# Optimization experiments

Measured on AMD Instinct MI355X. Metric: run time of the kernel, lower is better.

## Reference

```python
import jax, jax.numpy as jnp
import numpy as np

N_A = 50000; N_B = 50000          # nodes per type
FD = 8; BINS = 32; EMB = 16       # discrete features, bins, per-feature embed dim
HID = 64; ZD = 32                 # hidden_dim, embed_dim
E = 800000                        # edges per relation (avg degree 16)


def setup_inputs() -> dict:
    key = jax.random.key(0)
    ks = iter(jax.random.split(key, 64))
    def nrm(shape, s=0.05):
        return jax.random.normal(next(ks), shape, jnp.float32) * s
    def ri(shape, hi):
        return jax.random.randint(next(ks), shape, 0, hi, dtype=jnp.int32)
    inp = {
        'x_A': ri((N_A, FD), BINS),
        'x_B': ri((N_B, FD), BINS),
        'ei_ab': ri((2, E), N_A),   # src in A, dst in B (N_A == N_B)
        'ei_ba': ri((2, E), N_B),
        'ei_aa': ri((2, E), N_A),
        # per-feature embedding tables [FD, BINS, EMB]
        'emb_A': nrm((FD, BINS, EMB)), 'emb_B': nrm((FD, BINS, EMB)),
        # pre_lin per node type (in = FD*EMB)
        'pre_W_A': nrm((FD * EMB, HID)), 'pre_b_A': nrm((HID,)),
        'pre_W_B': nrm((FD * EMB, HID)), 'pre_b_B': nrm((HID,)),
        # SAGEConv per relation: lin_l (on aggregated msgs, with bias), lin_r (root, no bias)
        'sage_l_W_ab': nrm((HID, HID)), 'sage_l_b_ab': nrm((HID,)), 'sage_r_W_ab': nrm((HID, HID)),
        'sage_l_W_ba': nrm((HID, HID)), 'sage_l_b_ba': nrm((HID,)), 'sage_r_W_ba': nrm((HID, HID)),
        'sage_l_W_aa': nrm((HID, HID)), 'sage_l_b_aa': nrm((HID,)), 'sage_r_W_aa': nrm((HID, HID)),
        # lin_proj per node type
        'proj_W_A': nrm((HID, ZD)), 'proj_b_A': nrm((ZD,)),
        'proj_W_B': nrm((HID, ZD)), 'proj_b_B': nrm((ZD,)),
        # feature heads per node type -> FD*BINS logits
        'head_W_A': nrm((ZD, FD * BINS)), 'head_b_A': nrm((FD * BINS,)),
        'head_W_B': nrm((ZD, FD * BINS)), 'head_b_B': nrm((FD * BINS,)),
        # bilinear edge decoders per relation: W [1, ZD, ZD], bias [1]
        'bil_W_ab': nrm((1, ZD, ZD)), 'bil_b_ab': nrm((1,)),
        'bil_W_ba': nrm((1, ZD, ZD)), 'bil_b_ba': nrm((1,)),
        'bil_W_aa': nrm((1, ZD, ZD)), 'bil_b_aa': nrm((1,)),
    }
    return inp


def _segment_mean(vals, idx, n):
    s = jax.ops.segment_sum(vals, idx, num_segments=n)
    c = jax.ops.segment_sum(jnp.ones((vals.shape[0], 1), vals.dtype), idx, num_segments=n)
    return s / jnp.maximum(c, 1.0)


def _sage(x_src, x_dst, ei, Wl, bl, Wr):
    # SAGEConv: lin_l(mean_{j in N(i)} x_j) + lin_r(x_i)
    m = _segment_mean(x_src[ei[0]], ei[1], x_dst.shape[0])
    return m @ Wl + bl + x_dst @ Wr


def _embed(x, emb):
    # emb: [FD, BINS, EMB]; x: [N, FD] ints -> [N, FD*EMB]
    e = emb[jnp.arange(FD)[None, :], x]            # [N, FD, EMB]
    return e.reshape(x.shape[0], FD * EMB)


def _bilinear(zs, zd, W, b):
    # nn.Bilinear: out_o = zs^T W_o zd + b_o ; here out dim 1, squeeze
    return (jnp.einsum('ei,oij,ej->eo', zs, W, zd) + b)[:, 0]


def _forward(x_A, x_B, ei_ab, ei_ba, ei_aa,
             emb_A, emb_B, pre_W_A, pre_b_A, pre_W_B, pre_b_B,
             sage_l_W_ab, sage_l_b_ab, sage_r_W_ab,
             sage_l_W_ba, sage_l_b_ba, sage_r_W_ba,
             sage_l_W_aa, sage_l_b_aa, sage_r_W_aa,
             proj_W_A, proj_b_A, proj_W_B, proj_b_B,
             head_W_A, head_b_A, head_W_B, head_b_B,
             bil_W_ab, bil_b_ab, bil_W_ba, bil_b_ba, bil_W_aa, bil_b_aa):
    # feature encoder + pre_lin + relu
    x0_A = jax.nn.relu(_embed(x_A, emb_A) @ pre_W_A + pre_b_A)
    x0_B = jax.nn.relu(_embed(x_B, emb_B) @ pre_W_B + pre_b_B)
    # HeteroConv(SAGEConv per relation, aggr='mean' over relations per dst type)
    h_B = _sage(x0_A, x0_B, ei_ab, sage_l_W_ab, sage_l_b_ab, sage_r_W_ab)
    h_A = (_sage(x0_B, x0_A, ei_ba, sage_l_W_ba, sage_l_b_ba, sage_r_W_ba)
           + _sage(x0_A, x0_A, ei_aa, sage_l_W_aa, sage_l_b_aa, sage_r_W_aa)) * 0.5
    # projection
    z_A = jax.nn.relu(h_A @ proj_W_A + proj_b_A)
    z_B = jax.nn.relu(h_B @ proj_W_B + proj_b_B)
    # feature decode
    fl_A = (z_A @ head_W_A + head_b_A).reshape(-1, FD, BINS)
    fl_B = (z_B @ head_W_B + head_b_B).reshape(-1, FD, BINS)
    # edge decode (bilinear on gathered endpoint embeddings)
    s_ab = _bilinear(z_A[ei_ab[0]], z_B[ei_ab[1]], bil_W_ab, bil_b_ab)
    s_ba = _bilinear(z_B[ei_ba[0]], z_A[ei_ba[1]], bil_W_ba, bil_b_ba)
    s_aa = _bilinear(z_A[ei_aa[0]], z_A[ei_aa[1]], bil_W_aa, bil_b_aa)
    return (z_A, z_B, fl_A, fl_B, s_ab, s_ba, s_aa)


def reference(x_A, x_B, ei_ab, ei_ba, ei_aa,
              emb_A, emb_B, pre_W_A, pre_b_A, pre_W_B, pre_b_B,
              sage_l_W_ab, sage_l_b_ab, sage_r_W_ab,
              sage_l_W_ba, sage_l_b_ba, sage_r_W_ba,
              sage_l_W_aa, sage_l_b_aa, sage_r_W_aa,
              proj_W_A, proj_b_A, proj_W_B, proj_b_B,
              head_W_A, head_b_A, head_W_B, head_b_B,
              bil_W_ab, bil_b_ab, bil_W_ba, bil_b_ba, bil_W_aa, bil_b_aa):
    return _forward(x_A, x_B, ei_ab, ei_ba, ei_aa,
                    emb_A, emb_B, pre_W_A, pre_b_A, pre_W_B, pre_b_B,
                    sage_l_W_ab, sage_l_b_ab, sage_r_W_ab,
                    sage_l_W_ba, sage_l_b_ba, sage_r_W_ba,
                    sage_l_W_aa, sage_l_b_aa, sage_r_W_aa,
                    proj_W_A, proj_b_A, proj_W_B, proj_b_B,
                    head_W_A, head_b_A, head_W_B, head_b_B,
                    bil_W_ab, bil_b_ab, bil_W_ba, bil_b_ba, bil_W_aa, bil_b_aa)
```

## Files before the change

### kernel.cpp

```cpp
#include <hip/hip_runtime.h>

typedef unsigned short u16;
typedef unsigned int u32;
typedef __attribute__((ext_vector_type(8))) short short8;
typedef __attribute__((ext_vector_type(4))) float f32x4;

constexpr int NA = 50000, NB = 50000;
constexpr int EMB = 16, HID = 64;
constexpr int NE = 800000;
constexpr int NBKT = 782;
constexpr int CAPB = 1536;
constexpr int EPB = 2048;
constexpr int BPR = (NE + EPB - 1) / EPB;
constexpr int MSB = 3 * BPR;

#define MFMA16(a, b, c) __builtin_amdgcn_mfma_f32_16x16x32_bf16(a, b, c, 0, 0, 0)

__device__ inline u16 f2bf(float f) {
  u32 b = __float_as_uint(f);
  return (u16)((b + 0x7FFFu + ((b >> 16) & 1u)) >> 16);
}
__device__ inline float bfl(u32 u) { return __uint_as_float(u << 16); }
__device__ inline float bfh(u32 u) { return __uint_as_float(u & 0xFFFF0000u); }
__device__ inline float bfs(u16 u) { return __uint_as_float((u32)u << 16); }

__global__ void __launch_bounds__(256) k_pre(
    const float* __restrict__ embA, const float* __restrict__ embB,
    const float* __restrict__ preWA, const float* __restrict__ preWB,
    float* __restrict__ T,
    const float* __restrict__ Wr_ba, const float* __restrict__ Wr_aa,
    const float* __restrict__ Wl_ba, const float* __restrict__ Wl_aa,
    const float* __restrict__ Wl_ab, const float* __restrict__ Wr_ab,
    const float* __restrict__ bl_ba, const float* __restrict__ bl_aa,
    const float* __restrict__ projWA, const float* __restrict__ projWB,
    const float* __restrict__ headWA, const float* __restrict__ headWB,
    const float* __restrict__ bilW_ba, const float* __restrict__ bilW_aa,
    const float* __restrict__ bilW_ab,
    u16* __restrict__ frag, float* __restrict__ bhA,
    const int* __restrict__ ei_ab, const int* __restrict__ ei_ba,
    const int* __restrict__ ei_aa, int* __restrict__ gcur,
    u32* __restrict__ buckets) {
  __shared__ int hist[NBKT];
  __shared__ int wcur[NBKT];
  int blk = blockIdx.x;
  int t = threadIdx.x;

  if (blk < MSB) {
    int rel = blk / BPR;
    int lb = blk - rel * BPR;
    const int* ei = rel == 0 ? ei_ab : (rel == 1 ? ei_ba : ei_aa);
    int e0 = lb * EPB;
    int n = min(EPB, NE - e0);
    for (int i = t; i < NBKT; i += 256) hist[i] = 0;
    __syncthreads();
    for (int i = t; i < n; i += 256) {
      int dstn = ei[NE + e0 + i];
      atomicAdd(&hist[dstn >> 6], 1);
    }
    __syncthreads();
    for (int i = t; i < NBKT; i += 256) {
      int c = hist[i];
      wcur[i] = (c > 0) ? atomicAdd(&gcur[rel * NBKT + i], c) : 0;
    }
    __syncthreads();
    for (int i = t; i < n; i += 256) {
      int src = ei[e0 + i];
      int dstn = ei[NE + e0 + i];
      int b = dstn >> 6;
      int pos = atomicAdd(&wcur[b], 1);
      if (pos < CAPB)
        buckets[(size_t)(rel * NBKT + b) * CAPB + pos] =
            ((u32)src << 6) | (u32)(dstn & 63);
    }
    return;
  }

  if (blk < MSB + 128) {
    int id = (blk - MSB) * 256 + t;
    int type = id >> 14;
    int rem = id & 16383;
    int col = rem >> 8;
    int fdbin = rem & 255;
    int fd = fdbin >> 5;
    const float* emb = type ? embB : embA;
    const float* W = type ? preWB : preWA;
    const float* e = emb + fdbin * EMB;
    const float* w = W + (fd * EMB) * HID + col;
    float s = 0.f;
#pragma unroll
    for (int j = 0; j < EMB; ++j) s += e[j] * w[j * HID];
    T[id] = s;
    return;
  }

  int tid = (blk - MSB - 128) * 256 + t;
  if (tid >= 86 * 64) {
    int i = tid - 86 * 64;
    if (i < 64) bhA[i] = 0.5f * (bl_ba[i] + bl_aa[i]);
    return;
  }
  int f = tid >> 6, lane = tid & 63;
  int nidx = lane & 15, quad = lane >> 4;
  u16* dst = frag + (size_t)f * 512 + lane * 8;
#pragma unroll
  for (int j = 0; j < 8; ++j) {
    int kq = quad * 8 + j;
    float v;
    if (f < 24) {
      int s = f >> 2, nt = f & 3, k = s * 32 + kq, c = nt * 16 + nidx;
      v = (k < 64) ? 0.5f * (Wr_ba[k * 64 + c] + Wr_aa[k * 64 + c])
          : (k < 128) ? 0.5f * Wl_ba[(k - 64) * 64 + c]
                      : 0.5f * Wl_aa[(k - 128) * 64 + c];
    } else if (f < 28) {
      int g = f - 24, k = (g >> 1) * 32 + kq, c = (g & 1) * 16 + nidx;
      v = projWA[k * 32 + c];
    } else if (f < 44) {
      int c = (f - 28) * 16 + nidx;
      v = headWA[kq * 256 + c];
    } else if (f < 46) {
      int i2 = (f - 44) * 16 + nidx;
      v = bilW_ba[i2 * 32 + kq];
    } else if (f < 48) {
      int i2 = (f - 46) * 16 + nidx;
      v = bilW_aa[i2 * 32 + kq];
    } else if (f < 64) {
      int g = f - 48, s = g >> 2, nt = g & 3, k = s * 32 + kq, c = nt * 16 + nidx;
      v = (k < 64) ? Wr_ab[k * 64 + c] : Wl_ab[(k - 64) * 64 + c];
    } else if (f < 68) {
      int g = f - 64, k = (g >> 1) * 32 + kq, c = (g & 1) * 16 + nidx;
      v = projWB[k * 32 + c];
    } else if (f < 84) {
      int c = (f - 68) * 16 + nidx;
      v = headWB[kq * 256 + c];
    } else {
      int i2 = (f - 84) * 16 + nidx;
      v = bilW_ab[i2 * 32 + kq];
    }
    dst[j] = f2bf(v);
  }
}

__global__ void __launch_bounds__(256) k_x0(const int* __restrict__ xA,
                                            const int* __restrict__ xB,
                                            const float* __restrict__ T,
                                            const float* __restrict__ biasA,
                                            const float* __restrict__ biasB,
                                            u16* __restrict__ x0A,
                                            u16* __restrict__ x0B) {
  extern __shared__ float Tl[];
  int blk = blockIdx.x;
  int type = blk >= 782;
  int lb = type ? blk - 782 : blk;
  const int* x = type ? xB : xA;
  const float* Tt = T + (type ? 16384 : 0);
  const float* bias = type ? biasB : biasA;
  u16* x0 = type ? x0B : x0A;
  const int N = NA;

  const float4* Tg = (const float4*)Tt;
  float4* Ts = (float4*)Tl;
  for (int i = threadIdx.x; i < 4096; i += 256) {
    int col = i >> 6, b4 = i & 63;
    Ts[col * 64 + ((b4 + 2 * (col >> 4)) & 63)] = Tg[i];
  }
  __syncthreads();
  int t = threadIdx.x;
  int r = t >> 2, q = t & 3;
  int row = lb * 64 + r;
  bool valid = row < N;
  int arow = valid ? row : (N - 1);
  const int4* xp = (const int4*)(x + arow * 8);
  int4 xa = xp[0], xb = xp[1];
  int bins[8] = {xa.x, xa.y, xa.z, xa.w, xb.x, xb.y, xb.z, xb.w};
  int c0 = q * 16;
  float acc[16];
#pragma unroll
  for (int j = 0; j < 16; ++j) acc[j] = bias[c0 + j];
#pragma unroll
  for (int fd = 0; fd < 8; ++fd) {
    int sb = ((fd * 32 + bins[fd]) + 8 * q) & 255;
#pragma unroll
    for (int j = 0; j < 16; ++j) acc[j] += Tl[(c0 + j) * 256 + sb];
  }
  if (valid) {
    u32 p[8];
#pragma unroll
    for (int j = 0; j < 8; ++j) {
      u16 lo = f2bf(fmaxf(acc[2 * j], 0.f));
      u16 hi = f2bf(fmaxf(acc[2 * j + 1], 0.f));
      p[j] = (u32)lo | ((u32)hi << 16);
    }
    u32* o = (u32*)(x0 + (size_t)row * 64 + c0);
    *(uint4*)o = *(uint4*)&p[0];
    *((uint4*)o + 1) = *(uint4*)&p[4];
  }
}

__global__ void __launch_bounds__(256) k_meansort_all(
    const u32* __restrict__ buckets, const int* __restrict__ cur,
    const u16* __restrict__ x0A, const u16* __restrict__ x0B,
    u16* __restrict__ mab, u16* __restrict__ mba, u16* __restrict__ maa) {
  __shared__ u32 ebuf[CAPB];
  __shared__ u16 csr[CAPB];
  __shared__ int dcnt[64], doff[64], wcur[64];
  int blk = blockIdx.x;
  int rel = blk / NBKT;
  int lb = blk - rel * NBKT;
  int t = threadIdx.x;
  const u16* x0 = (rel == 1) ? x0B : x0A;
  u16* out = rel == 0 ? mab : (rel == 1 ? mba : maa);
  int n = min(cur[blk], CAPB);
  const u32* bk = buckets + (size_t)blk * CAPB;
  if (t < 64) dcnt[t] = 0;
  __syncthreads();
  for (int i = t; i < n; i += 256) {
    u32 v = bk[i];
    ebuf[i] = v;
    atomicAdd(&dcnt[v & 63], 1);
  }
  __syncthreads();
  if (t == 0) {
    int s = 0;
#pragma unroll
    for (int d = 0; d < 64; ++d) {
      doff[d] = s;
      wcur[d] = s;
      s += dcnt[d];
    }
  }
  __syncthreads();
  for (int i = t; i < n; i += 256) {
    u32 v = ebuf[i];
    int p = atomicAdd(&wcur[v & 63], 1);
    csr[p] = (u16)(v >> 6);
  }
  __syncthreads();
  int lane = t & 63, w = t >> 6;
  int g = lane >> 4;
  int dim4 = (lane & 15) * 4;
  int base = lb * 64;
  for (int c = 0; c < 4; ++c) {
    int dloc = w * 16 + c * 4 + g;
    int dstn = base + dloc;
    if (dstn < 50000) {
      int off = doff[dloc], deg = dcnt[dloc];
      float a0 = 0.f, a1 = 0.f, a2 = 0.f, a3 = 0.f;
      int i = 0;
      for (; i + 8 <= deg; i += 8) {
        uint2 v0 = *(const uint2*)(x0 + (size_t)csr[off + i] * 64 + dim4);
        uint2 v1 = *(const uint2*)(x0 + (size_t)csr[off + i + 1] * 64 + dim4);
        uint2 v2 = *(const uint2*)(x0 + (size_t)csr[off + i + 2] * 64 + dim4);
        uint2 v3 = *(const uint2*)(x0 + (size_t)csr[off + i + 3] * 64 + dim4);
        uint2 v4 = *(const uint2*)(x0 + (size_t)csr[off + i + 4] * 64 + dim4);
        uint2 v5 = *(const uint2*)(x0 + (size_t)csr[off + i + 5] * 64 + dim4);
        uint2 v6 = *(const uint2*)(x0 + (size_t)csr[off + i + 6] * 64 + dim4);
        uint2 v7 = *(const uint2*)(x0 + (size_t)csr[off + i + 7] * 64 + dim4);
        a0 += bfl(v0.x) + bfl(v1.x) + bfl(v2.x) + bfl(v3.x) +
              bfl(v4.x) + bfl(v5.x) + bfl(v6.x) + bfl(v7.x);
        a1 += bfh(v0.x) + bfh(v1.x) + bfh(v2.x) + bfh(v3.x) +
              bfh(v4.x) + bfh(v5.x) + bfh(v6.x) + bfh(v7.x);
        a2 += bfl(v0.y) + bfl(v1.y) + bfl(v2.y) + bfl(v3.y) +
              bfl(v4.y) + bfl(v5.y) + bfl(v6.y) + bfl(v7.y);
        a3 += bfh(v0.y) + bfh(v1.y) + bfh(v2.y) + bfh(v3.y) +
              bfh(v4.y) + bfh(v5.y) + bfh(v6.y) + bfh(v7.y);
      }
      for (; i + 4 <= deg; i += 4) {
        uint2 v0 = *(const uint2*)(x0 + (size_t)csr[off + i] * 64 + dim4);
        uint2 v1 = *(const uint2*)(x0 + (size_t)csr[off + i + 1] * 64 + dim4);
        uint2 v2 = *(const uint2*)(x0 + (size_t)csr[off + i + 2] * 64 + dim4);
        uint2 v3 = *(const uint2*)(x0 + (size_t)csr[off + i + 3] * 64 + dim4);
        a0 += bfl(v0.x) + bfl(v1.x) + bfl(v2.x) + bfl(v3.x);
        a1 += bfh(v0.x) + bfh(v1.x) + bfh(v2.x) + bfh(v3.x);
        a2 += bfl(v0.y) + bfl(v1.y) + bfl(v2.y) + bfl(v3.y);
        a3 += bfh(v0.y) + bfh(v1.y) + bfh(v2.y) + bfh(v3.y);
      }
      for (; i < deg; ++i) {
        uint2 v0 = *(const uint2*)(x0 + (size_t)csr[off + i] * 64 + dim4);
        a0 += bfl(v0.x);
        a1 += bfh(v0.x);
        a2 += bfl(v0.y);
        a3 += bfh(v0.y);
      }
      float inv = deg > 0 ? 1.f / (float)deg : 0.f;
      uint2 o;
      o.x = (u32)f2bf(a0 * inv) | ((u32)f2bf(a1 * inv) << 16);
      o.y = (u32)f2bf(a2 * inv) | ((u32)f2bf(a3 * inv) << 16);
      *(uint2*)(out + (size_t)dstn * 64 + dim4) = o;
    }
  }
}

template <int NS, int NY>
__device__ __forceinline__ void node_chain(
    const u16* __restrict__ x0, const u16* __restrict__ m1, const u16* __restrict__ m2,
    const u16* __restrict__ frag, int f1, int f2, int fy, int fh,
    const float* __restrict__ hbias, const float* __restrict__ projb,
    const float* __restrict__ headb,
    float* __restrict__ zout, float* __restrict__ flout,
    u16* __restrict__ zbf, u16* __restrict__ y1bf, u16* __restrict__ y2bf,
    int rows0, int N, u16* hld, u16* zld, int lane) {
  int nidx = lane & 15, quad = lane >> 4;
  size_t r0 = (size_t)min(rows0 + nidx, N - 1);
  size_t r1 = (size_t)min(rows0 + 16 + nidx, N - 1);

  f32x4 acc[2][4];
#pragma unroll
  for (int mt = 0; mt < 2; ++mt)
#pragma unroll
    for (int nt = 0; nt < 4; ++nt) acc[mt][nt] = {0.f, 0.f, 0.f, 0.f};
  const u16* mats[3] = {x0, m1, m2};
#pragma unroll
  for (int s = 0; s < NS; ++s) {
    const u16* src = mats[s >> 1];
    int koff = (s & 1) * 32 + quad * 8;
    short8 a0 = *(const short8*)(src + r0 * 64 + koff);
    short8 a1 = *(const short8*)(src + r1 * 64 + koff);
#pragma unroll
    for (int nt = 0; nt < 4; ++nt) {
      short8 b = *(const short8*)(frag + (size_t)(f1 + s * 4 + nt) * 512 + lane * 8);
      acc[0][nt] = MFMA16(a0, b, acc[0][nt]);
      acc[1][nt] = MFMA16(a1, b, acc[1][nt]);
    }
  }
#pragma unroll
  for (int mt = 0; mt < 2; ++mt)
#pragma unroll
    for (int nt = 0; nt < 4; ++nt) {
      int col = nt * 16 + nidx;
      float bb = hbias[col];
#pragma unroll
      for (int r2 = 0; r2 < 4; ++r2)
        hld[(mt * 16 + quad * 4 + r2) * 72 + col] = f2bf(acc[mt][nt][r2] + bb);
    }

  f32x4 zacc[2][2];
#pragma unroll
  for (int mt = 0; mt < 2; ++mt)
#pragma unroll
    for (int nt = 0; nt < 2; ++nt) zacc[mt][nt] = {0.f, 0.f, 0.f, 0.f};
#pragma unroll
  for (int s = 0; s < 2; ++s) {
    short8 a0 = *(const short8*)(hld + nidx * 72 + s * 32 + quad * 8);
    short8 a1 = *(const short8*)(hld + (16 + nidx) * 72 + s * 32 + quad * 8);
#pragma unroll
    for (int nt = 0; nt < 2; ++nt) {
      short8 b = *(const short8*)(frag + (size_t)(f2 + s * 2 + nt) * 512 + lane * 8);
      zacc[0][nt] = MFMA16(a0, b, zacc[0][nt]);
      zacc[1][nt] = MFMA16(a1, b, zacc[1][nt]);
    }
  }
#pragma unroll
  for (int mt = 0; mt < 2; ++mt)
#pragma unroll
    for (int nt = 0; nt < 2; ++nt) {
      int col = nt * 16 + nidx;
      float pb = projb[col];
#pragma unroll
      for (int r2 = 0; r2 < 4; ++r2) {
        int rl = mt * 16 + quad * 4 + r2;
        float zv = fmaxf(zacc[mt][nt][r2] + pb, 0.f);
        zld[rl * 40 + col] = f2bf(zv);
        int grow = rows0 + rl;
        if (grow < N) zout[(size_t)grow * 32 + col] = zv;
      }
    }
  {
    int rl = lane >> 1, hf = lane & 1;
    int grow = rows0 + rl;
    if (grow < N) {
      short8 v0 = *(const short8*)(zld + rl * 40 + hf * 16);
      short8 v1 = *(const short8*)(zld + rl * 40 + hf * 16 + 8);
      *(short8*)(zbf + (size_t)grow * 32 + hf * 16) = v0;
      *(short8*)(zbf + (size_t)grow * 32 + hf * 16 + 8) = v1;
    }
  }

  short8 az0 = *(const short8*)(zld + nidx * 40 + quad * 8);
  short8 az1 = *(const short8*)(zld + (16 + nidx) * 40 + quad * 8);
#pragma unroll
  for (int mat = 0; mat < NY; ++mat) {
    f32x4 ya[2][2];
#pragma unroll
    for (int mt = 0; mt < 2; ++mt)
#pragma unroll
      for (int nt = 0; nt < 2; ++nt) ya[mt][nt] = {0.f, 0.f, 0.f, 0.f};
#pragma unroll
    for (int nt = 0; nt < 2; ++nt) {
      short8 b = *(const short8*)(frag + (size_t)(fy + mat * 2 + nt) * 512 + lane * 8);
      ya[0][nt] = MFMA16(az0, b, ya[0][nt]);
      ya[1][nt] = MFMA16(az1, b, ya[1][nt]);
    }
#pragma unroll
    for (int mt = 0; mt < 2; ++mt)
#pragma unroll
      for (int nt = 0; nt < 2; ++nt)
#pragma unroll
        for (int r2 = 0; r2 < 4; ++r2)
          hld[(mt * 16 + quad * 4 + r2) * 40 + nt * 16 + nidx] = f2bf(ya[mt][nt][r2]);
    u16* yo = mat ? y2bf : y1bf;
    int rl = lane >> 1, hf = lane & 1;
    int grow = rows0 + rl;
    if (grow < N) {
      short8 v0 = *(const short8*)(hld + rl * 40 + hf * 16);
      short8 v1 = *(const short8*)(hld + rl * 40 + hf * 16 + 8);
      *(short8*)(yo + (size_t)grow * 32 + hf * 16) = v0;
      *(short8*)(yo + (size_t)grow * 32 + hf * 16 + 8) = v1;
    }
  }

  for (int chunk = 0; chunk < 4; ++chunk) {
    f32x4 fa[2][4];
#pragma unroll
    for (int mt = 0; mt < 2; ++mt)
#pragma unroll
      for (int nt = 0; nt < 4; ++nt) fa[mt][nt] = {0.f, 0.f, 0.f, 0.f};
#pragma unroll
    for (int nt = 0; nt < 4; ++nt) {
      short8 b = *(const short8*)(frag + (size_t)(fh + chunk * 4 + nt) * 512 + lane * 8);
      fa[0][nt] = MFMA16(az0, b, fa[0][nt]);
      fa[1][nt] = MFMA16(az1, b, fa[1][nt]);
    }
#pragma unroll
    for (int mt = 0; mt < 2; ++mt)
#pragma unroll
      for (int nt = 0; nt < 4; ++nt) {
        int col = chunk * 64 + nt * 16 + nidx;
        float hb = headb[col];
#pragma unroll
        for (int r2 = 0; r2 < 4; ++r2) {
          int grow = rows0 + mt * 16 + quad * 4 + r2;
          if (grow < N) flout[(size_t)grow * 256 + col] = fa[mt][nt][r2] + hb;
        }
      }
  }
}

__global__ void __launch_bounds__(256) k_node(
    const u16* __restrict__ x0A, const u16* __restrict__ mba, const u16* __restrict__ maa,
    const u16* __restrict__ x0B, const u16* __restrict__ mab,
    const u16* __restrict__ frag, const float* __restrict__ bhA,
    const float* __restrict__ bl_ab,
    const float* __restrict__ projbA, const float* __restrict__ headbA,
    const float* __restrict__ projbB, const float* __restrict__ headbB,
    float* __restrict__ zA, float* __restrict__ flA, u16* __restrict__ zAbf,
    u16* __restrict__ ybabf, u16* __restrict__ yaabf,
    float* __restrict__ zB, float* __restrict__ flB, u16* __restrict__ zBbf,
    u16* __restrict__ yabbf) {
  __shared__ u16 lds[4][3584];
  int t = threadIdx.x, lane = t & 63, w = t >> 6;
  u16* hld = &lds[w][0];
  u16* zld = &lds[w][2304];
  int blk = blockIdx.x;
  if (blk < 391) {
    node_chain<6, 2>(x0A, mba, maa, frag, 0, 24, 44, 28, bhA, projbA, headbA,
                     zA, flA, zAbf, ybabf, yaabf, blk * 128 + w * 32, NA, hld, zld, lane);
  } else {
    node_chain<4, 1>(x0B, mab, mab, frag, 48, 64, 84, 68, bl_ab, projbB, headbB,
                     zB, flB, zBbf, yabbf, yabbf, (blk - 391) * 128 + w * 32, NB, hld,
                     zld, lane);
  }
}

__global__ void __launch_bounds__(256) k_bil_all(
    const int* __restrict__ ei_ab, const int* __restrict__ ei_ba,
    const int* __restrict__ ei_aa,
    const u16* __restrict__ zA, const u16* __restrict__ zB,
    const u16* __restrict__ yab, const u16* __restrict__ yba,
    const u16* __restrict__ yaa,
    const float* __restrict__ b_ab, const float* __restrict__ b_ba,
    const float* __restrict__ b_aa,
    float* __restrict__ s_ab, float* __restrict__ s_ba,
    float* __restrict__ s_aa) {
  constexpr int NEH = NE / 2;
  int p = blockIdx.x * 256 + threadIdx.x;
  if (p >= 3 * NEH) return;
  int rel = p / NEH;
  int lp = p - rel * NEH;
  int le = 2 * lp;
  const int* ei = rel == 0 ? ei_ab : (rel == 1 ? ei_ba : ei_aa);
  const u16* zs = (rel == 1) ? zB : zA;
  const u16* yd = rel == 0 ? yab : (rel == 1 ? yba : yaa);
  const float* bb = rel == 0 ? b_ab : (rel == 1 ? b_ba : b_aa);
  float* so = rel == 0 ? s_ab : (rel == 1 ? s_ba : s_aa);
  int2 si = *(const int2*)(ei + le);
  int2 di = *(const int2*)(ei + NE + le);
  const uint4* zp0 = (const uint4*)(zs + (size_t)si.x * 32);
  const uint4* yp0 = (const uint4*)(yd + (size_t)di.x * 32);
  const uint4* zp1 = (const uint4*)(zs + (size_t)si.y * 32);
  const uint4* yp1 = (const uint4*)(yd + (size_t)di.y * 32);
  float acc0 = 0.f, acc1 = 0.f;
#pragma unroll
  for (int i = 0; i < 4; ++i) {
    uint4 a0 = zp0[i], c0 = yp0[i];
    uint4 a1 = zp1[i], c1 = yp1[i];
    acc0 += bfl(a0.x) * bfl(c0.x) + bfh(a0.x) * bfh(c0.x);
    acc0 += bfl(a0.y) * bfl(c0.y) + bfh(a0.y) * bfh(c0.y);
    acc0 += bfl(a0.z) * bfl(c0.z) + bfh(a0.z) * bfh(c0.z);
    acc0 += bfl(a0.w) * bfl(c0.w) + bfh(a0.w) * bfh(c0.w);
    acc1 += bfl(a1.x) * bfl(c1.x) + bfh(a1.x) * bfh(c1.x);
    acc1 += bfl(a1.y) * bfl(c1.y) + bfh(a1.y) * bfh(c1.y);
    acc1 += bfl(a1.z) * bfl(c1.z) + bfh(a1.z) * bfh(c1.z);
    acc1 += bfl(a1.w) * bfl(c1.w) + bfh(a1.w) * bfh(c1.w);
  }
  float2 o;
  o.x = acc0 + bb[0];
  o.y = acc1 + bb[0];
  *(float2*)(so + le) = o;
}

extern "C" void kernel_launch(void* const* d_in, const int* in_sizes, int n_in,
                              void* d_out, int out_size, void* d_ws, size_t ws_size,
                              hipStream_t stream) {
  const int* xA = (const int*)d_in[0];
  const int* xB = (const int*)d_in[1];
  const int* ei_ab = (const int*)d_in[2];
  const int* ei_ba = (const int*)d_in[3];
  const int* ei_aa = (const int*)d_in[4];
  const float* embA = (const float*)d_in[5];
  const float* embB = (const float*)d_in[6];
  const float* preWA = (const float*)d_in[7];
  const float* prebA = (const float*)d_in[8];
  const float* preWB = (const float*)d_in[9];
  const float* prebB = (const float*)d_in[10];
  const float* Wl_ab = (const float*)d_in[11];
  const float* bl_ab = (const float*)d_in[12];
  const float* Wr_ab = (const float*)d_in[13];
  const float* Wl_ba = (const float*)d_in[14];
  const float* bl_ba = (const float*)d_in[15];
  const float* Wr_ba = (const float*)d_in[16];
  const float* Wl_aa = (const float*)d_in[17];
  const float* bl_aa = (const float*)d_in[18];
  const float* Wr_aa = (const float*)d_in[19];
  const float* projWA = (const float*)d_in[20];
  const float* projbA = (const float*)d_in[21];
  const float* projWB = (const float*)d_in[22];
  const float* projbB = (const float*)d_in[23];
  const float* headWA = (const float*)d_in[24];
  const float* headbA = (const float*)d_in[25];
  const float* headWB = (const float*)d_in[26];
  const float* headbB = (const float*)d_in[27];
  const float* bilW_ab = (const float*)d_in[28];
  const float* bilb_ab = (const float*)d_in[29];
  const float* bilW_ba = (const float*)d_in[30];
  const float* bilb_ba = (const float*)d_in[31];
  const float* bilW_aa = (const float*)d_in[32];
  const float* bilb_aa = (const float*)d_in[33];

  float* out = (float*)d_out;
  float* zA = out;
  float* zB = out + 1600000;
  float* flA = out + 3200000;
  float* flB = out + 16000000;
  float* s_ab = out + 28800000;
  float* s_ba = out + 29600000;
  float* s_aa = out + 30400000;

  char* ws = (char*)d_ws;
  float* T = (float*)(ws + 0);
  u16* x0Abf = (u16*)(ws + 131072);
  u16* x0Bbf = (u16*)(ws + 6531072);
  u16* mabbf = (u16*)(ws + 12931072);
  u16* mbabf = (u16*)(ws + 19331072);
  u16* maabf = (u16*)(ws + 25731072);
  u16* zAbf = (u16*)(ws + 32131072);
  u16* zBbf = (u16*)(ws + 35331072);
  u16* yabbf = (u16*)(ws + 38531072);
  u16* ybabf = (u16*)(ws + 41731072);
  u16* yaabf = (u16*)(ws + 44931072);
  int* cur = (int*)(ws + 48131072);
  u16* frag = (u16*)(ws + 48731072);
  float* bhA = (float*)(ws + 48819136);

  u32* buckets = (u32*)flA;

  hipMemsetAsync(cur, 0, 3 * NBKT * sizeof(int), stream);
  k_pre<<<MSB + 150, 256, 0, stream>>>(
      embA, embB, preWA, preWB, T,
      Wr_ba, Wr_aa, Wl_ba, Wl_aa, Wl_ab, Wr_ab, bl_ba, bl_aa,
      projWA, projWB, headWA, headWB, bilW_ba, bilW_aa, bilW_ab,
      frag, bhA, ei_ab, ei_ba, ei_aa, cur, buckets);
  k_x0<<<2 * 782, 256, 65536, stream>>>(xA, xB, T, prebA, prebB, x0Abf, x0Bbf);
  k_meansort_all<<<3 * NBKT, 256, 0, stream>>>(buckets, cur, x0Abf, x0Bbf,
                                               mabbf, mbabf, maabf);
  k_node<<<782, 256, 0, stream>>>(x0Abf, mbabf, maabf, x0Bbf, mabbf, frag, bhA,
                                  bl_ab, projbA, headbA, projbB, headbB,
                                  zA, flA, zAbf, ybabf, yaabf, zB, flB, zBbf, yabbf);
  k_bil_all<<<(3 * (NE / 2) + 255) / 256, 256, 0, stream>>>(
      ei_ab, ei_ba, ei_aa, zAbf, zBbf, yabbf, ybabf, yaabf,
      bilb_ab, bilb_ba, bilb_aa, s_ab, s_ba, s_aa);
}
```

Before: 435.2 us.

## Map bilinear scoring blocks to relations by XCD, one edge per thread

The edge bilinear scoring kernel now assigns blocks to relations by blockIdx mod 8. Since blocks are dispatched round-robin over the chiplets, each chiplet works on a single relation, and the gathered z/y rows it reads should stay in that chiplet's L2 cache. Each thread now scores one edge instead of two, which doubles the grid size. The trade-off is less memory-level parallelism per thread and a slightly uneven split between the relations (3/3/2 chiplets). The speedup also depends on the hardware's block-to-chiplet dispatch order.

Measured after the change: 411.4 us. -5.5%, faster.

```diff
diff --git a/kernel.cpp b/kernel.cpp
--- a/kernel.cpp
+++ b/kernel.cpp
@@ -471,41 +471,35 @@
     const float* __restrict__ b_aa,
     float* __restrict__ s_ab, float* __restrict__ s_ba,
     float* __restrict__ s_aa) {
-  constexpr int NEH = NE / 2;
-  int p = blockIdx.x * 256 + threadIdx.x;
-  if (p >= 3 * NEH) return;
-  int rel = p / NEH;
-  int lp = p - rel * NEH;
-  int le = 2 * lp;
+  constexpr int NCHUNK = NE / 256;
+  int blk = blockIdx.x;
+  int c = blk & 7;
+  int o = blk >> 3;
+  int rel, cb, ncls;
+  if (c < 3) { rel = 0; cb = 0; ncls = 3; }
+  else if (c < 6) { rel = 1; cb = 3; ncls = 3; }
+  else { rel = 2; cb = 6; ncls = 2; }
+  int chunk = (c - cb) + ncls * o;
+  if (chunk >= NCHUNK) return;
+  int le = chunk * 256 + threadIdx.x;
   const int* ei = rel == 0 ? ei_ab : (rel == 1 ? ei_ba : ei_aa);
   const u16* zs = (rel == 1) ? zB : zA;
   const u16* yd = rel == 0 ? yab : (rel == 1 ? yba : yaa);
   const float* bb = rel == 0 ? b_ab : (rel == 1 ? b_ba : b_aa);
   float* so = rel == 0 ? s_ab : (rel == 1 ? s_ba : s_aa);
-  int2 si = *(const int2*)(ei + le);
-  int2 di = *(const int2*)(ei + NE + le);
-  const uint4* zp0 = (const uint4*)(zs + (size_t)si.x * 32);
-  const uint4* yp0 = (const uint4*)(yd + (size_t)di.x * 32);
-  const uint4* zp1 = (const uint4*)(zs + (size_t)si.y * 32);
-  const uint4* yp1 = (const uint4*)(yd + (size_t)di.y * 32);
-  float acc0 = 0.f, acc1 = 0.f;
+  int si = ei[le], di = ei[NE + le];
+  const uint4* zp = (const uint4*)(zs + (size_t)si * 32);
+  const uint4* yp = (const uint4*)(yd + (size_t)di * 32);
+  float acc = 0.f;
 #pragma unroll
   for (int i = 0; i < 4; ++i) {
-    uint4 a0 = zp0[i], c0 = yp0[i];
-    uint4 a1 = zp1[i], c1 = yp1[i];
-    acc0 += bfl(a0.x) * bfl(c0.x) + bfh(a0.x) * bfh(c0.x);
-    acc0 += bfl(a0.y) * bfl(c0.y) + bfh(a0.y) * bfh(c0.y);
-    acc0 += bfl(a0.z) * bfl(c0.z) + bfh(a0.z) * bfh(c0.z);
-    acc0 += bfl(a0.w) * bfl(c0.w) + bfh(a0.w) * bfh(c0.w);
-    acc1 += bfl(a1.x) * bfl(c1.x) + bfh(a1.x) * bfh(c1.x);
-    acc1 += bfl(a1.y) * bfl(c1.y) + bfh(a1.y) * bfh(c1.y);
-    acc1 += bfl(a1.z) * bfl(c1.z) + bfh(a1.z) * bfh(c1.z);
-    acc1 += bfl(a1.w) * bfl(c1.w) + bfh(a1.w) * bfh(c1.w);
-  }
-  float2 o;
-  o.x = acc0 + bb[0];
-  o.y = acc1 + bb[0];
-  *(float2*)(so + le) = o;
+    uint4 a = zp[i], cc = yp[i];
+    acc += bfl(a.x) * bfl(cc.x) + bfh(a.x) * bfh(cc.x);
+    acc += bfl(a.y) * bfl(cc.y) + bfh(a.y) * bfh(cc.y);
+    acc += bfl(a.z) * bfl(cc.z) + bfh(a.z) * bfh(cc.z);
+    acc += bfl(a.w) * bfl(cc.w) + bfh(a.w) * bfh(cc.w);
+  }
+  so[le] = acc + bb[0];
 }
 
 extern "C" void kernel_launch(void* const* d_in, const int* in_sizes, int n_in,
@@ -585,7 +579,7 @@
   k_node<<<782, 256, 0, stream>>>(x0Abf, mbabf, maabf, x0Bbf, mabbf, frag, bhA,
                                   bl_ab, projbA, headbA, projbB, headbB,
                                   zA, flA, zAbf, ybabf, yaabf, zB, flB, zBbf, yabbf);
-  k_bil_all<<<(3 * (NE / 2) + 255) / 256, 256, 0, stream>>>(
+  k_bil_all<<<8 * 1563, 256, 0, stream>>>(
       ei_ab, ei_ba, ei_aa, zAbf, zBbf, yabbf, ybabf, yaabf,
       bilb_ab, bilb_ba, bilb_aa, s_ab, s_ba, s_aa);
 }
```
